# Optimization experiments

Hardware: AMD Instinct MI355X
Metric: run time of the kernel (lower is better)

Reference implementation:

```python
import jax, jax.numpy as jnp
import numpy as np

B, SX, SY, H = 4, 512, 512, 128


def setup_inputs() -> dict:
    key = jax.random.key(0)
    k1, k2, k3, k4, k5 = jax.random.split(key, 5)
    x = jax.random.normal(k1, (B, SX, 2 * H), dtype=jnp.float32)
    y = jax.random.normal(k2, (B, SY, 2 * H), dtype=jnp.float32)
    # nn.Linear(in, out, bias=False) weight has shape (out, in)
    s = 1.0 / np.sqrt(2 * H)
    Wc1 = jax.random.uniform(k3, (H, 2 * H), minval=-s, maxval=s, dtype=jnp.float32)
    Wc2 = jax.random.uniform(k4, (H, 2 * H), minval=-s, maxval=s, dtype=jnp.float32)
    sv = 1.0 / np.sqrt(H)
    vc = jax.random.uniform(k5, (1, H), minval=-sv, maxval=sv, dtype=jnp.float32)
    return {"x": x, "y": y, "Wc1": Wc1, "Wc2": Wc2, "vc": vc}


def reference(x, y, Wc1, Wc2, vc):
    # s1: (B, Sx, H), s2: (B, Sy, H)
    s1 = jnp.einsum('bsd,hd->bsh', x, Wc1)
    s2 = jnp.einsum('btd,hd->bth', y, Wc2)
    # broadcast tanh-MLP score: (B, Sy, Sx, H) -> (B, Sy, Sx)
    sjt = jnp.einsum('btsh,h->bts', jnp.tanh(s1[:, None, :, :] + s2[:, :, None, :]), vc[0])
    ait = jax.nn.softmax(sjt, axis=2)  # softmax over Sx
    qtc = jnp.einsum('bts,bsd->btd', ait, x)  # (B, Sy, 2H)
    return qtc
```

## Files before the change

kernel.cpp:

```cpp
#include <hip/hip_runtime.h>


#define NB 4
#define SEQ 512
#define HDIM 128
#define DDIM 256

static constexpr float TWO_LOG2E = 2.8853900817779268f;
static constexpr float LOG2E     = 1.4426950408889634f;

__global__ __launch_bounds__(256) void wtrans_kernel(
    const float* __restrict__ W1, const float* __restrict__ W2,
    float* __restrict__ Wt1, float* __restrict__ Wt2)
{
    __shared__ float sT[32 * 132];
    const int blk = blockIdx.x;
    const int which = blk >> 3;
    const int s = blk & 7;
    const float* W  = which ? W2 : W1;
    float*       Wt = which ? Wt2 : Wt1;
    const int tid = threadIdx.x;

    #pragma unroll
    for (int i = 0; i < 4; ++i) {
        const int idx = i * 256 + tid;
        const int h = idx >> 3, k4 = idx & 7;
        const float4 v = ((const float4*)W)[h * 64 + s * 8 + k4];
        sT[(k4 * 4 + 0) * 132 + h] = v.x;
        sT[(k4 * 4 + 1) * 132 + h] = v.y;
        sT[(k4 * 4 + 2) * 132 + h] = v.z;
        sT[(k4 * 4 + 3) * 132 + h] = v.w;
    }
    __syncthreads();
    #pragma unroll
    for (int i = 0; i < 4; ++i) {
        const int idx = i * 256 + tid;
        const int kl = idx >> 5, hq = idx & 31;
        float4 o;
        o.x = sT[kl * 132 + 4 * hq + 0];
        o.y = sT[kl * 132 + 4 * hq + 1];
        o.z = sT[kl * 132 + 4 * hq + 2];
        o.w = sT[kl * 132 + 4 * hq + 3];
        ((float4*)Wt)[(s * 32 + kl) * 32 + hq] = o;
    }
}

__global__ __launch_bounds__(256) void proj_kernel(
    const float* __restrict__ x, const float* __restrict__ y,
    const float* __restrict__ Wt1, const float* __restrict__ Wt2,
    float* __restrict__ e1sw, float* __restrict__ e2)
{
    __shared__ float As[2048];
    __shared__ float sPr[8192];
    const int tid = threadIdx.x;
    const int gr0 = blockIdx.x * 8;

    const float* in; const float* Wt; int srow;
    if (gr0 < 2048) { in = x; Wt = Wt1; srow = gr0; }
    else            { in = y; Wt = Wt2; srow = gr0 - 2048; }

    #pragma unroll
    for (int j = 0; j < 2; ++j) {
        const int idx = tid + j * 256;
        const int r = idx >> 6, kk = idx & 63;
        *(float4*)&As[idx * 4] =
            *(const float4*)&in[(srow + r) * 256 + kk * 4];
    }
    __syncthreads();

    const int hq = tid & 31;
    const int ks = tid >> 5;
    const float4* Wt4 = (const float4*)Wt;

    float4 acc4[8];
    #pragma unroll
    for (int r = 0; r < 8; ++r) acc4[r] = make_float4(0.f, 0.f, 0.f, 0.f);

    #pragma unroll
    for (int u = 0; u < 8; ++u) {
        const int kof = ks * 32 + u * 4;
        const float4 w0 = Wt4[(kof + 0) * 32 + hq];
        const float4 w1 = Wt4[(kof + 1) * 32 + hq];
        const float4 w2 = Wt4[(kof + 2) * 32 + hq];
        const float4 w3 = Wt4[(kof + 3) * 32 + hq];
        #pragma unroll
        for (int r = 0; r < 8; ++r) {
            const float4 a = *(const float4*)&As[r * 256 + kof];
            acc4[r].x = fmaf(a.w,w3.x, fmaf(a.z,w2.x, fmaf(a.y,w1.x, fmaf(a.x,w0.x, acc4[r].x))));
            acc4[r].y = fmaf(a.w,w3.y, fmaf(a.z,w2.y, fmaf(a.y,w1.y, fmaf(a.x,w0.y, acc4[r].y))));
            acc4[r].z = fmaf(a.w,w3.z, fmaf(a.z,w2.z, fmaf(a.y,w1.z, fmaf(a.x,w0.z, acc4[r].z))));
            acc4[r].w = fmaf(a.w,w3.w, fmaf(a.z,w2.w, fmaf(a.y,w1.w, fmaf(a.x,w0.w, acc4[r].w))));
        }
    }
    #pragma unroll
    for (int r = 0; r < 8; ++r)
        *(float4*)&sPr[ks * 1024 + r * 128 + hq * 4] = acc4[r];
    __syncthreads();
    {
        const int r = tid >> 5, h4 = tid & 31;
        float4 s = make_float4(0.f, 0.f, 0.f, 0.f);
        #pragma unroll
        for (int k2 = 0; k2 < 8; ++k2) {
            const float4 p = *(const float4*)&sPr[k2 * 1024 + r * 128 + h4 * 4];
            s.x += p.x; s.y += p.y; s.z += p.z; s.w += p.w;
        }
        float4 o;
        o.x = __builtin_amdgcn_exp2f(s.x * TWO_LOG2E);
        o.y = __builtin_amdgcn_exp2f(s.y * TWO_LOG2E);
        o.z = __builtin_amdgcn_exp2f(s.z * TWO_LOG2E);
        o.w = __builtin_amdgcn_exp2f(s.w * TWO_LOG2E);
        const int gr = gr0 + r;
        if (gr < 2048) {
            const int b = gr >> 9, ss = gr & 511;
            const int c = ss >> 6, sl = ss & 63;
            ((float4*)e1sw)[((b * 8 + c) * 32 + h4) * 64 + (sl ^ h4)] = o;
        } else {
            ((float4*)e2)[(gr - 2048) * 32 + h4] = o;
        }
    }
}

__global__ __launch_bounds__(1024) void score_kernel(
    const float* __restrict__ e1sw, const float* __restrict__ e2g,
    const float* __restrict__ vc,  float* __restrict__ P)
{
    __shared__ float sPartC[2][16 * 256];
    __shared__ float sScore[4 * 512];

    const int tid  = threadIdx.x;
    const int b    = blockIdx.x >> 7;
    const int t0   = (blockIdx.x & 127) * 4;
    const int w    = tid >> 6;
    const int lane = tid & 63;
    const int wu   = __builtin_amdgcn_readfirstlane(w);
    const int hg   = wu;

    float4 vcs[2];
    float4 e2s[4][2];
    #pragma unroll
    for (int j = 0; j < 2; ++j)
        vcs[j] = *(const float4*)&vc[(hg * 2 + j) * 4];
    #pragma unroll
    for (int t = 0; t < 4; ++t)
        #pragma unroll
        for (int j = 0; j < 2; ++j)
            e2s[t][j] = *(const float4*)&e2g[(b * SEQ + t0 + t) * HDIM + (hg * 2 + j) * 4];

    const float4* e1c = (const float4*)e1sw + b * 16384;

    for (int c = 0; c < 8; ++c) {
        const float4* chunk = e1c + c * 2048;
        float acc0 = 0.f, acc1 = 0.f, acc2 = 0.f, acc3 = 0.f;
        #pragma unroll
        for (int j = 0; j < 2; ++j) {
            const int hq = hg * 2 + j;
            const float4 e1 = chunk[hq * 64 + (lane ^ hq)];
            const float4 vv = vcs[j];
            #pragma unroll
            for (int t = 0; t < 4; ++t) {
                const float4 e2 = e2s[t][j];
                const float f1 = fmaf(e1.x, e2.x, 1.f);
                const float f2 = fmaf(e1.y, e2.y, 1.f);
                const float f3 = fmaf(e1.z, e2.z, 1.f);
                const float f4 = fmaf(e1.w, e2.w, 1.f);
                const float f12 = f1 * f2, f34 = f3 * f4;
                const float n12 = fmaf(vv.x, f2, vv.y * f1);
                const float n34 = fmaf(vv.z, f4, vv.w * f3);
                const float num = fmaf(n12, f34, n34 * f12);
                const float r = fmaf(num, __builtin_amdgcn_rcpf(f12 * f34),
                                     (t == 0) ? acc0 : (t == 1) ? acc1 : (t == 2) ? acc2 : acc3);
                if      (t == 0) acc0 = r;
                else if (t == 1) acc1 = r;
                else if (t == 2) acc2 = r;
                else             acc3 = r;
            }
        }
        float* pb = sPartC[c & 1] + wu * 256 + lane;
        pb[0 * 64] = acc0;
        pb[1 * 64] = acc1;
        pb[2 * 64] = acc2;
        pb[3 * 64] = acc3;
        __syncthreads();
        if (tid < 256) {
            const int t = tid >> 6, s = tid & 63;
            const float* pc = sPartC[c & 1] + t * 64 + s;
            float r = 0.f;
            #pragma unroll
            for (int ww = 0; ww < 16; ++ww) r += pc[ww * 256];
            sScore[t * 512 + c * 64 + s] = -2.f * r;
        }
    }
    __syncthreads();

    if (w < 4) {
        float v[8];
        float m = -1e30f;
        #pragma unroll
        for (int j = 0; j < 8; ++j) {
            v[j] = sScore[w * 512 + lane + j * 64];
            m = fmaxf(m, v[j]);
        }
        #pragma unroll
        for (int off = 32; off; off >>= 1) m = fmaxf(m, __shfl_xor(m, off));
        float sum = 0.f;
        #pragma unroll
        for (int j = 0; j < 8; ++j) {
            v[j] = __builtin_amdgcn_exp2f((v[j] - m) * LOG2E);
            sum += v[j];
        }
        #pragma unroll
        for (int off = 32; off; off >>= 1) sum += __shfl_xor(sum, off);
        const float inv = __builtin_amdgcn_rcpf(sum);
        float* Prow = &P[(b * SEQ + t0 + w) * SEQ];
        #pragma unroll
        for (int j = 0; j < 8; ++j)
            Prow[lane + j * 64] = v[j] * inv;
    }
}

__global__ __launch_bounds__(512) void pax_kernel(
    const float* __restrict__ P, const float* __restrict__ x,
    float* __restrict__ out)
{
    __shared__ float sP[SEQ * 8];
    __shared__ float sRed[8 * 8 * DDIM];
    const int tid = threadIdx.x;
    const int b   = blockIdx.x >> 6;
    const int t0  = (blockIdx.x & 63) * 8;
    const int w    = tid >> 6;
    const int lane = tid & 63;

    #pragma unroll
    for (int j = 0; j < 2; ++j) {
        const int i = tid + j * 512;
        const int t = i >> 7, c4 = i & 127;
        const float4 p = *(const float4*)&P[(b * SEQ + t0 + t) * SEQ + c4 * 4];
        sP[(c4 * 4 + 0) * 8 + t] = p.x;
        sP[(c4 * 4 + 1) * 8 + t] = p.y;
        sP[(c4 * 4 + 2) * 8 + t] = p.z;
        sP[(c4 * 4 + 3) * 8 + t] = p.w;
    }
    __syncthreads();

    const float4* x4 = (const float4*)x;
    float4 acc[8];
    #pragma unroll
    for (int t = 0; t < 8; ++t) acc[t] = make_float4(0.f, 0.f, 0.f, 0.f);

    #pragma unroll 4
    for (int si = 0; si < 64; ++si) {
        const int s = w * 64 + si;
        const float4 xv  = x4[(b * SEQ + s) * 64 + lane];
        const float4 p03 = *(const float4*)&sP[s * 8];
        const float4 p47 = *(const float4*)&sP[s * 8 + 4];
        acc[0].x = fmaf(p03.x, xv.x, acc[0].x); acc[0].y = fmaf(p03.x, xv.y, acc[0].y);
        acc[0].z = fmaf(p03.x, xv.z, acc[0].z); acc[0].w = fmaf(p03.x, xv.w, acc[0].w);
        acc[1].x = fmaf(p03.y, xv.x, acc[1].x); acc[1].y = fmaf(p03.y, xv.y, acc[1].y);
        acc[1].z = fmaf(p03.y, xv.z, acc[1].z); acc[1].w = fmaf(p03.y, xv.w, acc[1].w);
        acc[2].x = fmaf(p03.z, xv.x, acc[2].x); acc[2].y = fmaf(p03.z, xv.y, acc[2].y);
        acc[2].z = fmaf(p03.z, xv.z, acc[2].z); acc[2].w = fmaf(p03.z, xv.w, acc[2].w);
        acc[3].x = fmaf(p03.w, xv.x, acc[3].x); acc[3].y = fmaf(p03.w, xv.y, acc[3].y);
        acc[3].z = fmaf(p03.w, xv.z, acc[3].z); acc[3].w = fmaf(p03.w, xv.w, acc[3].w);
        acc[4].x = fmaf(p47.x, xv.x, acc[4].x); acc[4].y = fmaf(p47.x, xv.y, acc[4].y);
        acc[4].z = fmaf(p47.x, xv.z, acc[4].z); acc[4].w = fmaf(p47.x, xv.w, acc[4].w);
        acc[5].x = fmaf(p47.y, xv.x, acc[5].x); acc[5].y = fmaf(p47.y, xv.y, acc[5].y);
        acc[5].z = fmaf(p47.y, xv.z, acc[5].z); acc[5].w = fmaf(p47.y, xv.w, acc[5].w);
        acc[6].x = fmaf(p47.z, xv.x, acc[6].x); acc[6].y = fmaf(p47.z, xv.y, acc[6].y);
        acc[6].z = fmaf(p47.z, xv.z, acc[6].z); acc[6].w = fmaf(p47.z, xv.w, acc[6].w);
        acc[7].x = fmaf(p47.w, xv.x, acc[7].x); acc[7].y = fmaf(p47.w, xv.y, acc[7].y);
        acc[7].z = fmaf(p47.w, xv.z, acc[7].z); acc[7].w = fmaf(p47.w, xv.w, acc[7].w);
    }
    __syncthreads();
    float4* sRed4 = (float4*)sRed;
    #pragma unroll
    for (int t = 0; t < 8; ++t)
        sRed4[w * 512 + t * 64 + lane] = acc[t];
    __syncthreads();
    #pragma unroll
    for (int j = 0; j < 4; ++j) {
        const int i = tid + j * 512;
        const int t = i >> 8, d = i & 255;
        const float r = sRed[0*2048 + t*256 + d] + sRed[1*2048 + t*256 + d]
                      + sRed[2*2048 + t*256 + d] + sRed[3*2048 + t*256 + d]
                      + sRed[4*2048 + t*256 + d] + sRed[5*2048 + t*256 + d]
                      + sRed[6*2048 + t*256 + d] + sRed[7*2048 + t*256 + d];
        out[(b * SEQ + t0 + t) * DDIM + d] = r;
    }
}

extern "C" void kernel_launch(void* const* d_in, const int* in_sizes, int n_in,
                              void* d_out, int out_size, void* d_ws, size_t ws_size,
                              hipStream_t stream) {
    const float* x   = (const float*)d_in[0];
    const float* y   = (const float*)d_in[1];
    const float* W1  = (const float*)d_in[2];
    const float* W2  = (const float*)d_in[3];
    const float* vc  = (const float*)d_in[4];
    float* outp = (float*)d_out;

    float* ws  = (float*)d_ws;
    float* e1  = ws;
    float* e2  = ws + NB * SEQ * HDIM;
    float* P   = ws + 2 * NB * SEQ * HDIM;
    float* Wt1 = P + NB * SEQ * SEQ;
    float* Wt2 = Wt1 + HDIM * DDIM;

    hipLaunchKernelGGL(wtrans_kernel, dim3(16),  dim3(256),  0, stream,
                       W1, W2, Wt1, Wt2);
    hipLaunchKernelGGL(proj_kernel,   dim3(512), dim3(256),  0, stream,
                       x, y, Wt1, Wt2, e1, e2);
    hipLaunchKernelGGL(score_kernel,  dim3(512), dim3(1024), 0, stream,
                       e1, e2, vc, P);
    hipLaunchKernelGGL(pax_kernel,    dim3(256), dim3(512),  0, stream,
                       P, x, outp);
}
```

Baseline: 99.34 us.

## Prefetch e1 chunks, halve score barriers, double pax_kernel threads

In score_kernel, the e1 loads for the next chunk are issued before the current chunk is computed. The partial sums are double-buffered across chunk pairs, so one barrier and one reduction cover two chunks instead of one. pax_kernel moves to 1024 threads with 16 waves splitting the sequence. Its cross-wave reduction becomes a two-stage add through shared memory, which is meant to add latency hiding and occupancy. The cost is more registers for the prefetched values and an extra barrier stage in pax.

New measurement: 97.98 us. About the same (-1.4%).

```diff
diff --git a/kernel.cpp b/kernel.cpp
--- a/kernel.cpp
+++ b/kernel.cpp
@@ -124,7 +124,7 @@
     const float* __restrict__ e1sw, const float* __restrict__ e2g,
     const float* __restrict__ vc,  float* __restrict__ P)
 {
-    __shared__ float sPartC[2][16 * 256];
+    __shared__ float sPartC[2][2][16 * 256];
     __shared__ float sScore[4 * 512];
 
     const int tid  = threadIdx.x;
@@ -148,13 +148,23 @@
 
     const float4* e1c = (const float4*)e1sw + b * 16384;
 
+    const int off0 = (hg * 2 + 0) * 64 + (lane ^ (hg * 2 + 0));
+    const int off1 = (hg * 2 + 1) * 64 + (lane ^ (hg * 2 + 1));
+
+    float4 e1v0 = e1c[off0];
+    float4 e1v1 = e1c[off1];
+
     for (int c = 0; c < 8; ++c) {
-        const float4* chunk = e1c + c * 2048;
+        float4 e1n0 = e1v0, e1n1 = e1v1;
+        if (c < 7) {
+            const float4* nx = e1c + (c + 1) * 2048;
+            e1n0 = nx[off0];
+            e1n1 = nx[off1];
+        }
         float acc0 = 0.f, acc1 = 0.f, acc2 = 0.f, acc3 = 0.f;
         #pragma unroll
         for (int j = 0; j < 2; ++j) {
-            const int hq = hg * 2 + j;
-            const float4 e1 = chunk[hq * 64 + (lane ^ hq)];
+            const float4 e1 = j ? e1v1 : e1v0;
             const float4 vv = vcs[j];
             #pragma unroll
             for (int t = 0; t < 4; ++t) {
@@ -175,20 +185,25 @@
                 else             acc3 = r;
             }
         }
-        float* pb = sPartC[c & 1] + wu * 256 + lane;
+        float* pb = &sPartC[(c >> 1) & 1][c & 1][0] + wu * 256 + lane;
         pb[0 * 64] = acc0;
         pb[1 * 64] = acc1;
         pb[2 * 64] = acc2;
         pb[3 * 64] = acc3;
-        __syncthreads();
-        if (tid < 256) {
-            const int t = tid >> 6, s = tid & 63;
-            const float* pc = sPartC[c & 1] + t * 64 + s;
-            float r = 0.f;
-            #pragma unroll
-            for (int ww = 0; ww < 16; ++ww) r += pc[ww * 256];
-            sScore[t * 512 + c * 64 + s] = -2.f * r;
-        }
+        if (c & 1) {
+            __syncthreads();
+            if (tid < 512) {
+                const int ch = tid >> 8;
+                const int t  = (tid >> 6) & 3, s = tid & 63;
+                const float* pc = &sPartC[(c >> 1) & 1][ch][0] + t * 64 + s;
+                float r = 0.f;
+                #pragma unroll
+                for (int ww = 0; ww < 16; ++ww) r += pc[ww * 256];
+                sScore[t * 512 + (c - 1 + ch) * 64 + s] = -2.f * r;
+            }
+        }
+        e1v0 = e1n0;
+        e1v1 = e1n1;
     }
     __syncthreads();
 
@@ -218,7 +233,7 @@
     }
 }
 
-__global__ __launch_bounds__(512) void pax_kernel(
+__global__ __launch_bounds__(1024) void pax_kernel(
     const float* __restrict__ P, const float* __restrict__ x,
     float* __restrict__ out)
 {
@@ -230,10 +245,8 @@
     const int w    = tid >> 6;
     const int lane = tid & 63;
 
-    #pragma unroll
-    for (int j = 0; j < 2; ++j) {
-        const int i = tid + j * 512;
-        const int t = i >> 7, c4 = i & 127;
+    {
+        const int t = tid >> 7, c4 = tid & 127;
         const float4 p = *(const float4*)&P[(b * SEQ + t0 + t) * SEQ + c4 * 4];
         sP[(c4 * 4 + 0) * 8 + t] = p.x;
         sP[(c4 * 4 + 1) * 8 + t] = p.y;
@@ -248,8 +261,8 @@
     for (int t = 0; t < 8; ++t) acc[t] = make_float4(0.f, 0.f, 0.f, 0.f);
 
     #pragma unroll 4
-    for (int si = 0; si < 64; ++si) {
-        const int s = w * 64 + si;
+    for (int si = 0; si < 32; ++si) {
+        const int s = w * 32 + si;
         const float4 xv  = x4[(b * SEQ + s) * 64 + lane];
         const float4 p03 = *(const float4*)&sP[s * 8];
         const float4 p47 = *(const float4*)&sP[s * 8 + 4];
@@ -270,20 +283,30 @@
         acc[7].x = fmaf(p47.w, xv.x, acc[7].x); acc[7].y = fmaf(p47.w, xv.y, acc[7].y);
         acc[7].z = fmaf(p47.w, xv.z, acc[7].z); acc[7].w = fmaf(p47.w, xv.w, acc[7].w);
     }
-    __syncthreads();
+
     float4* sRed4 = (float4*)sRed;
-    #pragma unroll
-    for (int t = 0; t < 8; ++t)
-        sRed4[w * 512 + t * 64 + lane] = acc[t];
-    __syncthreads();
-    #pragma unroll
-    for (int j = 0; j < 4; ++j) {
-        const int i = tid + j * 512;
+    if (w < 8) {
+        #pragma unroll
+        for (int t = 0; t < 8; ++t)
+            sRed4[w * 512 + t * 64 + lane] = acc[t];
+    }
+    __syncthreads();
+    if (w >= 8) {
+        #pragma unroll
+        for (int t = 0; t < 8; ++t) {
+            float4 r = sRed4[(w - 8) * 512 + t * 64 + lane];
+            r.x += acc[t].x; r.y += acc[t].y; r.z += acc[t].z; r.w += acc[t].w;
+            sRed4[(w - 8) * 512 + t * 64 + lane] = r;
+        }
+    }
+    __syncthreads();
+    #pragma unroll
+    for (int j = 0; j < 2; ++j) {
+        const int i = tid + j * 1024;
         const int t = i >> 8, d = i & 255;
-        const float r = sRed[0*2048 + t*256 + d] + sRed[1*2048 + t*256 + d]
-                      + sRed[2*2048 + t*256 + d] + sRed[3*2048 + t*256 + d]
-                      + sRed[4*2048 + t*256 + d] + sRed[5*2048 + t*256 + d]
-                      + sRed[6*2048 + t*256 + d] + sRed[7*2048 + t*256 + d];
+        float r = 0.f;
+        #pragma unroll
+        for (int q = 0; q < 8; ++q) r += sRed[q * 2048 + t * 256 + d];
         out[(b * SEQ + t0 + t) * DDIM + d] = r;
     }
 }
@@ -311,6 +334,6 @@
                        x, y, Wt1, Wt2, e1, e2);
     hipLaunchKernelGGL(score_kernel,  dim3(512), dim3(1024), 0, stream,
                        e1, e2, vc, P);
-    hipLaunchKernelGGL(pax_kernel,    dim3(256), dim3(512),  0, stream,
+    hipLaunchKernelGGL(pax_kernel,    dim3(256), dim3(1024), 0, stream,
                        P, x, outp);
 }
```
